# Kernel optimization log

Measured on AMD Instinct MI355X. Metric: run time of the kernel, lower is better.

The kernel has to match this reference:

```python
import jax, jax.numpy as jnp
import numpy as np

N = 131072      # total nodes
B = 512         # number of graphs
F_DIM = 512     # in_channels
H = F_DIM // 2  # score_net hidden
RATIO = 0.5
MARGIN = 0.5
TOPK_LOSS_WEIGHT = 0.2


def setup_inputs() -> dict:
    key = jax.random.key(0)
    k1, k2, k3 = jax.random.split(key, 3)
    x = jax.random.normal(k1, (N, F_DIM), dtype=jnp.float32)
    # sorted segment ids: equal-sized graphs of N // B nodes
    batch = (jnp.arange(N) // (N // B)).astype(jnp.int32)
    W1 = jax.random.normal(k2, (F_DIM, H), dtype=jnp.float32) / np.sqrt(F_DIM).astype(np.float32)
    b1 = jnp.zeros((H,), dtype=jnp.float32)
    W2 = jax.random.normal(k3, (H, 1), dtype=jnp.float32) / np.sqrt(H).astype(np.float32)
    b2 = jnp.zeros((1,), dtype=jnp.float32)
    return {"x": x, "batch": batch, "W1": W1, "b1": b1, "W2": W2, "b2": b2}


def reference(x, batch, W1, b1, W2, b2):
    # scores = score_net(x).squeeze(-1)   [N]
    scores = (jax.nn.relu(x @ W1 + b1) @ W2 + b2)[:, 0]

    # per-graph node counts and k = max(1, int(ratio * n_i))
    counts = jax.ops.segment_sum(jnp.ones((N,), dtype=scores.dtype), batch, num_segments=B)
    k = jnp.maximum(1, jnp.floor(RATIO * counts).astype(jnp.int32))  # [B]

    # segmented top-k via lexsort: sort by (batch asc, score desc)
    order = jnp.lexsort((-scores, batch))          # [N] permutation
    b_sorted = batch[order]
    starts = jnp.cumsum(counts) - counts           # exclusive-cumsum segment starts
    rank = jnp.arange(N, dtype=counts.dtype) - starts[b_sorted]  # rank within graph (0 = highest score)
    sel_sorted = rank < k[b_sorted].astype(counts.dtype)
    selected_mask = jnp.zeros((N,), dtype=bool).at[order].set(sel_sorted)

    # global_add_pool over selected nodes
    m = selected_mask.astype(x.dtype)
    x_pooled = jax.ops.segment_sum(x * m[:, None], batch, num_segments=B)  # [B, F]

    # margin regularization loss per graph
    sel_cnt = jax.ops.segment_sum(m, batch, num_segments=B)
    sel_sum = jax.ops.segment_sum(scores * m, batch, num_segments=B)
    tot_sum = jax.ops.segment_sum(scores, batch, num_segments=B)
    uns_cnt = counts - sel_cnt
    sel_mean = sel_sum / jnp.maximum(sel_cnt, 1.0)
    uns_mean = (tot_sum - sel_sum) / jnp.maximum(uns_cnt, 1.0)
    per_graph = jnp.where(uns_cnt > 0, jax.nn.relu(MARGIN - (sel_mean - uns_mean)), 0.0)
    topk_loss = per_graph.sum() / B * TOPK_LOSS_WEIGHT

    return x_pooled, topk_loss, selected_mask
```

## Files before the change

### kernel.cpp

```cpp
#include <hip/hip_runtime.h>

#define BGRAPHS 512
#define FDIM    512
#define HDIM    256
#define NPG     256
#define KSEL    128
#define STAGES  16
#define BSTAGE_SHORTS 16384
#define A_ROW   40
#define A_PLANE (NPG * A_ROW)

typedef __attribute__((ext_vector_type(8)))  _Float16 f16x8;
typedef __attribute__((ext_vector_type(8)))  short    s16x8;
typedef __attribute__((ext_vector_type(16))) float    f32x16;

__device__ __forceinline__ unsigned short f16_rne(float f, float* back) {
    _Float16 h = (_Float16)f;
    *back = (float)h;
    union { _Float16 h; unsigned short s; } cv; cv.h = h;
    return cv.s;
}

__global__ __launch_bounds__(256)
void split_w1_kernel(const float* __restrict__ W1, unsigned short* __restrict__ wsB)
{
    const int uid  = blockIdx.x * 256 + threadIdx.x;
    const int lane = uid & 63;
    int t = uid >> 6;
    const int nt = t & 7;  t >>= 3;
    const int p  = t & 1;  t >>= 1;
    const int q  = t & 1;
    const int s  = t >> 1;
    const int n  = nt * 32 + (lane & 31);
    const int k0 = s * 32 + q * 16 + (lane >> 5) * 8;

    s16x8 v;
    #pragma unroll
    for (int j = 0; j < 8; ++j) {
        float w = W1[(size_t)(k0 + j) * HDIM + n] * 1024.0f;
        float f1, f2;
        unsigned short h1 = f16_rne(w, &f1);
        unsigned short h2 = f16_rne(w - f1, &f2);
        v[j] = (short)(p ? h2 : h1);
    }
    *(s16x8*)(wsB + (size_t)uid * 8) = v;
}

__global__ __launch_bounds__(512, 2)
void fused_kernel(const float* __restrict__ x,
                  const unsigned short* __restrict__ wsB,
                  const float* __restrict__ b1, const float* __restrict__ W2,
                  const float* __restrict__ b2,
                  float* __restrict__ pooled, float* __restrict__ mask_out,
                  float* __restrict__ loss_per_g)
{
    __shared__ __attribute__((aligned(16))) unsigned char smem[147456];

    const int g    = blockIdx.x;
    const int tid  = threadIdx.x;
    const int lane = tid & 63;
    const int wv   = tid >> 6;
    const int wy   = wv & 3;
    const int wx   = wv >> 2;
    const int l31  = lane & 31;
    const int lh   = lane >> 5;

    const int c     = tid & 7;
    const int rbase = tid >> 3;
    const float* aptr = x + ((size_t)(g * NPG + rbase)) * FDIM + c * 4;

    f32x16 acc[2][4];
    #pragma unroll
    for (int a = 0; a < 2; ++a)
        #pragma unroll
        for (int b = 0; b < 4; ++b)
            #pragma unroll
            for (int rr = 0; rr < 16; ++rr) acc[a][b][rr] = 0.f;

    float4 aA0, aA1, aA2, aA3;
    float4 aB0, aB1, aB2, aB3;

#define GLL_B(S1) do {                                                          \
    const unsigned short* _src = wsB + (size_t)(S1) * BSTAGE_SHORTS;            \
    unsigned short* _dst = (unsigned short*)smem + ((S1) & 1) * BSTAGE_SHORTS;  \
    _Pragma("unroll")                                                           \
    for (int _i = 0; _i < 4; ++_i) {                                            \
        const int _u = _i * 512 + tid;                                          \
        __builtin_amdgcn_global_load_lds(                                       \
            (const __attribute__((address_space(1))) unsigned int*)(_src + (size_t)_u * 8), \
            (__attribute__((address_space(3))) unsigned int*)(_dst + _u * 8),   \
            16, 0, 0);                                                          \
    } } while (0)

#define LOAD_PF(P0,P1,P2,P3,S2) do {                                            \
    const float* _ap = aptr + (S2) * 32;                                        \
    P0 = *(const float4*)(_ap + 0 * 64 * FDIM);                                 \
    P1 = *(const float4*)(_ap + 1 * 64 * FDIM);                                 \
    P2 = *(const float4*)(_ap + 2 * 64 * FDIM);                                 \
    P3 = *(const float4*)(_ap + 3 * 64 * FDIM); } while (0)

#define CONV1(P,KK,BUF) do {                                                    \
    float _f[4] = {P.x, P.y, P.z, P.w};                                         \
    unsigned short _H[4], _M[4];                                                \
    _Pragma("unroll")                                                           \
    for (int _j = 0; _j < 4; ++_j) {                                            \
        float _b1v, _b2v;                                                       \
        float _xs = _f[_j] * 64.0f;                            \
        _H[_j] = f16_rne(_xs, &_b1v);                                           \
        _M[_j] = f16_rne(_xs - _b1v, &_b2v);                                    \
        (void)_b2v;                                                             \
    }                                                                           \
    unsigned short* _pl = (unsigned short*)(smem + 65536 + (BUF) * 40960)       \
                          + (rbase + 64 * (KK)) * A_ROW + c * 4;                \
    uint2 _uH, _uM;                                                             \
    _uH.x = (unsigned)_H[0] | ((unsigned)_H[1] << 16);                          \
    _uH.y = (unsigned)_H[2] | ((unsigned)_H[3] << 16);                          \
    _uM.x = (unsigned)_M[0] | ((unsigned)_M[1] << 16);                          \
    _uM.y = (unsigned)_M[2] | ((unsigned)_M[3] << 16);                          \
    *(uint2*)_pl = _uH;                                                         \
    *(uint2*)(_pl + A_PLANE) = _uM;                                             \
    } while (0)

#define CONVERT_A(P0,P1,P2,P3,BUF) do {                                         \
    CONV1(P0, 0, BUF); CONV1(P1, 1, BUF);                                       \
    CONV1(P2, 2, BUF); CONV1(P3, 3, BUF); } while (0)

#define COMPUTE(BUF) do {                                                       \
    const f16x8* _bfp = (const f16x8*)(smem + (BUF) * (BSTAGE_SHORTS * 2));     \
    const unsigned short* _aB = (const unsigned short*)(smem + 65536 + (BUF) * 40960); \
    _Pragma("unroll")                                                           \
    for (int _q = 0; _q < 2; ++_q) {                                            \
        const int _a0 = (wy * 64 + l31) * A_ROW + _q * 16 + lh * 8;             \
        const int _a1 = _a0 + 32 * A_ROW;                                       \
        f16x8 A0h = *(const f16x8*)(_aB + _a0);                                 \
        f16x8 A0m = *(const f16x8*)(_aB + A_PLANE + _a0);                       \
        f16x8 A1h = *(const f16x8*)(_aB + _a1);                                 \
        f16x8 A1m = *(const f16x8*)(_aB + A_PLANE + _a1);                       \
        _Pragma("unroll")                                                       \
        for (int _nt = 0; _nt < 4; ++_nt) {                                     \
            const int _nn = wx * 4 + _nt;                                       \
            f16x8 Bh = _bfp[((_q * 2 + 0) * 8 + _nn) * 64 + lane];              \
            f16x8 Bm = _bfp[((_q * 2 + 1) * 8 + _nn) * 64 + lane];              \
            acc[0][_nt] = __builtin_amdgcn_mfma_f32_32x32x16_f16(A0h, Bh, acc[0][_nt], 0, 0, 0); \
            acc[1][_nt] = __builtin_amdgcn_mfma_f32_32x32x16_f16(A1h, Bh, acc[1][_nt], 0, 0, 0); \
            acc[0][_nt] = __builtin_amdgcn_mfma_f32_32x32x16_f16(A0m, Bh, acc[0][_nt], 0, 0, 0); \
            acc[1][_nt] = __builtin_amdgcn_mfma_f32_32x32x16_f16(A1m, Bh, acc[1][_nt], 0, 0, 0); \
            acc[0][_nt] = __builtin_amdgcn_mfma_f32_32x32x16_f16(A0h, Bm, acc[0][_nt], 0, 0, 0); \
            acc[1][_nt] = __builtin_amdgcn_mfma_f32_32x32x16_f16(A1h, Bm, acc[1][_nt], 0, 0, 0); \
        }                                                                       \
    } } while (0)

    LOAD_PF(aA0, aA1, aA2, aA3, 0);
    GLL_B(0);
    CONVERT_A(aA0, aA1, aA2, aA3, 0);
    LOAD_PF(aA0, aA1, aA2, aA3, 1);
    __syncthreads();

    for (int s = 0; s < STAGES; s += 2) {
        if (s < STAGES - 1) GLL_B(s + 1);
        if (s < STAGES - 2) LOAD_PF(aB0, aB1, aB2, aB3, s + 2);
        COMPUTE(0);
        if (s < STAGES - 1) CONVERT_A(aA0, aA1, aA2, aA3, 1);
        __syncthreads();

        if (s + 1 < STAGES - 1) GLL_B(s + 2);
        if (s + 1 < STAGES - 2) LOAD_PF(aA0, aA1, aA2, aA3, s + 3);
        COMPUTE(1);
        if (s + 1 < STAGES - 1) CONVERT_A(aB0, aB1, aB2, aB3, 0);
        __syncthreads();
    }

    float* Sp   = (float*)smem;
    float* sv   = Sp + 2 * NPG;
    int*   selr = (int*)(sv + NPG);
    float* redT = (float*)(selr + KSEL);
    float* redS = redT + NPG;

    float bb[4], ww[4];
    #pragma unroll
    for (int nt = 0; nt < 4; ++nt) {
        const int cc = wx * 128 + nt * 32 + l31;
        bb[nt] = b1[cc];
        ww[nt] = W2[cc];
    }
    const float unscale = 1.0f / 65536.0f;
    #pragma unroll
    for (int mt = 0; mt < 2; ++mt) {
        float pr[16];
        #pragma unroll
        for (int rr = 0; rr < 16; ++rr) pr[rr] = 0.f;
        #pragma unroll
        for (int nt = 0; nt < 4; ++nt)
            #pragma unroll
            for (int rr = 0; rr < 16; ++rr) {
                float h = fmaf(acc[mt][nt][rr], unscale, bb[nt]);
                h = h > 0.f ? h : 0.f;
                pr[rr] = fmaf(h, ww[nt], pr[rr]);
            }
        #pragma unroll
        for (int mask = 1; mask <= 16; mask <<= 1)
            #pragma unroll
            for (int rr = 0; rr < 16; ++rr)
                pr[rr] += __shfl_xor(pr[rr], mask);
        if (l31 == 0) {
            #pragma unroll
            for (int rr = 0; rr < 16; ++rr) {
                const int row = wy * 64 + mt * 32 + (rr & 3) + 8 * (rr >> 2) + 4 * lh;
                Sp[wx * NPG + row] = pr[rr];
            }
        }
    }
    __syncthreads();

    float sc = 0.f;
    if (tid < NPG) {
        sc = b2[0] + Sp[tid] + Sp[NPG + tid];
        sv[tid] = sc;
    }
    __syncthreads();

    if (tid < NPG) {
        int rank = 0;
        for (int j = 0; j < NPG; ++j) {
            const float sj = sv[j];
            rank += (sj > sc || (sj == sc && j < tid)) ? 1 : 0;
        }
        const bool sel = rank < KSEL;
        mask_out[g * NPG + tid] = sel ? 1.0f : 0.0f;
        if (sel) selr[rank] = tid;
        redT[tid] = sc;
        redS[tid] = sel ? sc : 0.f;
    }
    __syncthreads();

    for (int off = 128; off > 0; off >>= 1) {
        if (tid < off) { redT[tid] += redT[tid + off]; redS[tid] += redS[tid + off]; }
        __syncthreads();
    }
    if (tid == 0) {
        const float tot = redT[0], ssum = redS[0];
        const float sel_mean = ssum * (1.0f / KSEL);
        const float uns_mean = (tot - ssum) * (1.0f / (NPG - KSEL));
        const float v = 0.5f - (sel_mean - uns_mean);
        loss_per_g[g] = v > 0.f ? v : 0.f;
    }

    const int col = tid;
    const float* __restrict__ xg = x + (size_t)g * NPG * FDIM;
    float a0 = 0.f, a1 = 0.f, a2 = 0.f, a3 = 0.f;
    float a4 = 0.f, a5 = 0.f, a6 = 0.f, a7 = 0.f;
    #pragma unroll 2
    for (int n = 0; n < KSEL; n += 8) {
        a0 += xg[(size_t)selr[n + 0] * FDIM + col];
        a1 += xg[(size_t)selr[n + 1] * FDIM + col];
        a2 += xg[(size_t)selr[n + 2] * FDIM + col];
        a3 += xg[(size_t)selr[n + 3] * FDIM + col];
        a4 += xg[(size_t)selr[n + 4] * FDIM + col];
        a5 += xg[(size_t)selr[n + 5] * FDIM + col];
        a6 += xg[(size_t)selr[n + 6] * FDIM + col];
        a7 += xg[(size_t)selr[n + 7] * FDIM + col];
    }
    pooled[g * FDIM + col] = ((a0 + a1) + (a2 + a3)) + ((a4 + a5) + (a6 + a7));

#undef GLL_B
#undef LOAD_PF
#undef CONV1
#undef CONVERT_A
#undef COMPUTE
}

__global__ __launch_bounds__(256)
void loss_kernel(const float* __restrict__ loss_per_g, float* __restrict__ out_loss)
{
    __shared__ float red[256];
    const int t = threadIdx.x;
    red[t] = loss_per_g[t] + loss_per_g[t + 256];
    __syncthreads();
    for (int off = 128; off > 0; off >>= 1) {
        if (t < off) red[t] += red[t + off];
        __syncthreads();
    }
    if (t == 0) out_loss[0] = red[0] * (0.2f / BGRAPHS);
}

extern "C" void kernel_launch(void* const* d_in, const int* in_sizes, int n_in,
                              void* d_out, int out_size, void* d_ws, size_t ws_size,
                              hipStream_t stream)
{
    const float* x  = (const float*)d_in[0];
    const float* W1 = (const float*)d_in[2];
    const float* b1 = (const float*)d_in[3];
    const float* W2 = (const float*)d_in[4];
    const float* b2 = (const float*)d_in[5];

    float* out    = (float*)d_out;
    float* pooled = out;
    float* loss   = out + BGRAPHS * FDIM;
    float* mask   = loss + 1;

    float* loss_g       = (float*)d_ws;
    unsigned short* wsB = (unsigned short*)((char*)d_ws + 4096);

    split_w1_kernel<<<128, 256, 0, stream>>>(W1, wsB);
    fused_kernel<<<BGRAPHS, 512, 0, stream>>>(x, wsB, b1, W2, b2,
                                              pooled, mask, loss_g);
    loss_kernel<<<1, 256, 0, stream>>>(loss_g, loss);
}
```

Measured before the change: 417.3 us.

## Split fused kernel into half-graph GEMM and separate select/pool kernels

```diff
diff --git a/kernel.cpp b/kernel.cpp
--- a/kernel.cpp
+++ b/kernel.cpp
@@ -5,10 +5,10 @@
 #define HDIM    256
 #define NPG     256
 #define KSEL    128
-#define STAGES  16
-#define BSTAGE_SHORTS 16384
-#define A_ROW   40
-#define A_PLANE (NPG * A_ROW)
+#define STAGES  32
+#define BSTAGE_SHORTS 8192
+#define A_ROW   24
+#define A_PLANE (128 * A_ROW)
 
 typedef __attribute__((ext_vector_type(8)))  _Float16 f16x8;
 typedef __attribute__((ext_vector_type(8)))  short    s16x8;
@@ -29,10 +29,9 @@
     int t = uid >> 6;
     const int nt = t & 7;  t >>= 3;
     const int p  = t & 1;  t >>= 1;
-    const int q  = t & 1;
-    const int s  = t >> 1;
+    const int s  = t;
     const int n  = nt * 32 + (lane & 31);
-    const int k0 = s * 32 + q * 16 + (lane >> 5) * 8;
+    const int k0 = s * 16 + (lane >> 5) * 8;
 
     s16x8 v;
     #pragma unroll
@@ -46,45 +45,45 @@
     *(s16x8*)(wsB + (size_t)uid * 8) = v;
 }
 
-__global__ __launch_bounds__(512, 2)
-void fused_kernel(const float* __restrict__ x,
-                  const unsigned short* __restrict__ wsB,
-                  const float* __restrict__ b1, const float* __restrict__ W2,
-                  const float* __restrict__ b2,
-                  float* __restrict__ pooled, float* __restrict__ mask_out,
-                  float* __restrict__ loss_per_g)
-{
-    __shared__ __attribute__((aligned(16))) unsigned char smem[147456];
-
-    const int g    = blockIdx.x;
+__global__ __launch_bounds__(512, 4)
+void gemm_kernel(const float* __restrict__ x,
+                 const unsigned short* __restrict__ wsB,
+                 const float* __restrict__ b1, const float* __restrict__ W2,
+                 const float* __restrict__ b2,
+                 float* __restrict__ scores_out)
+{
+    __shared__ __attribute__((aligned(16))) unsigned char smem[57344];
+
+    const int bid  = blockIdx.x;
+    const int g    = bid >> 1;
+    const int rh   = bid & 1;
     const int tid  = threadIdx.x;
     const int lane = tid & 63;
     const int wv   = tid >> 6;
-    const int wy   = wv & 3;
-    const int wx   = wv >> 2;
+    const int wy   = wv & 1;
+    const int wx   = wv >> 1;
     const int l31  = lane & 31;
     const int lh   = lane >> 5;
 
-    const int c     = tid & 7;
-    const int rbase = tid >> 3;
-    const float* aptr = x + ((size_t)(g * NPG + rbase)) * FDIM + c * 4;
-
-    f32x16 acc[2][4];
+    const int arow  = tid >> 2;
+    const int achk  = tid & 3;
+    const float* aptr = x + ((size_t)(g * NPG + rh * 128 + arow)) * FDIM + achk * 4;
+
+    f32x16 acc[2][2];
     #pragma unroll
     for (int a = 0; a < 2; ++a)
         #pragma unroll
-        for (int b = 0; b < 4; ++b)
+        for (int b = 0; b < 2; ++b)
             #pragma unroll
             for (int rr = 0; rr < 16; ++rr) acc[a][b][rr] = 0.f;
 
-    float4 aA0, aA1, aA2, aA3;
-    float4 aB0, aB1, aB2, aB3;
+    float4 aA, aB;
 
 #define GLL_B(S1) do {                                                          \
     const unsigned short* _src = wsB + (size_t)(S1) * BSTAGE_SHORTS;            \
     unsigned short* _dst = (unsigned short*)smem + ((S1) & 1) * BSTAGE_SHORTS;  \
     _Pragma("unroll")                                                           \
-    for (int _i = 0; _i < 4; ++_i) {                                            \
+    for (int _i = 0; _i < 2; ++_i) {                                            \
         const int _u = _i * 512 + tid;                                          \
         __builtin_amdgcn_global_load_lds(                                       \
             (const __attribute__((address_space(1))) unsigned int*)(_src + (size_t)_u * 8), \
@@ -92,14 +91,9 @@
             16, 0, 0);                                                          \
     } } while (0)
 
-#define LOAD_PF(P0,P1,P2,P3,S2) do {                                            \
-    const float* _ap = aptr + (S2) * 32;                                        \
-    P0 = *(const float4*)(_ap + 0 * 64 * FDIM);                                 \
-    P1 = *(const float4*)(_ap + 1 * 64 * FDIM);                                 \
-    P2 = *(const float4*)(_ap + 2 * 64 * FDIM);                                 \
-    P3 = *(const float4*)(_ap + 3 * 64 * FDIM); } while (0)
-
-#define CONV1(P,KK,BUF) do {                                                    \
+#define LOAD_PF(P,S2) do { P = *(const float4*)(aptr + (S2) * 16); } while (0)
+
+#define CONVERT_A(P,BUF) do {                                                   \
     float _f[4] = {P.x, P.y, P.z, P.w};                                         \
     unsigned short _H[4], _M[4];                                                \
     _Pragma("unroll")                                                           \
@@ -110,8 +104,8 @@
         _M[_j] = f16_rne(_xs - _b1v, &_b2v);                                    \
         (void)_b2v;                                                             \
     }                                                                           \
-    unsigned short* _pl = (unsigned short*)(smem + 65536 + (BUF) * 40960)       \
-                          + (rbase + 64 * (KK)) * A_ROW + c * 4;                \
+    unsigned short* _pl = (unsigned short*)(smem + 32768 + (BUF) * 12288)       \
+                          + arow * A_ROW + achk * 4;                            \
     uint2 _uH, _uM;                                                             \
     _uH.x = (unsigned)_H[0] | ((unsigned)_H[1] << 16);                          \
     _uH.y = (unsigned)_H[2] | ((unsigned)_H[3] << 16);                          \
@@ -121,65 +115,59 @@
     *(uint2*)(_pl + A_PLANE) = _uM;                                             \
     } while (0)
 
-#define CONVERT_A(P0,P1,P2,P3,BUF) do {                                         \
-    CONV1(P0, 0, BUF); CONV1(P1, 1, BUF);                                       \
-    CONV1(P2, 2, BUF); CONV1(P3, 3, BUF); } while (0)
-
 #define COMPUTE(BUF) do {                                                       \
     const f16x8* _bfp = (const f16x8*)(smem + (BUF) * (BSTAGE_SHORTS * 2));     \
-    const unsigned short* _aB = (const unsigned short*)(smem + 65536 + (BUF) * 40960); \
-    _Pragma("unroll")                                                           \
-    for (int _q = 0; _q < 2; ++_q) {                                            \
-        const int _a0 = (wy * 64 + l31) * A_ROW + _q * 16 + lh * 8;             \
-        const int _a1 = _a0 + 32 * A_ROW;                                       \
-        f16x8 A0h = *(const f16x8*)(_aB + _a0);                                 \
-        f16x8 A0m = *(const f16x8*)(_aB + A_PLANE + _a0);                       \
-        f16x8 A1h = *(const f16x8*)(_aB + _a1);                                 \
-        f16x8 A1m = *(const f16x8*)(_aB + A_PLANE + _a1);                       \
-        _Pragma("unroll")                                                       \
-        for (int _nt = 0; _nt < 4; ++_nt) {                                     \
-            const int _nn = wx * 4 + _nt;                                       \
-            f16x8 Bh = _bfp[((_q * 2 + 0) * 8 + _nn) * 64 + lane];              \
-            f16x8 Bm = _bfp[((_q * 2 + 1) * 8 + _nn) * 64 + lane];              \
-            acc[0][_nt] = __builtin_amdgcn_mfma_f32_32x32x16_f16(A0h, Bh, acc[0][_nt], 0, 0, 0); \
-            acc[1][_nt] = __builtin_amdgcn_mfma_f32_32x32x16_f16(A1h, Bh, acc[1][_nt], 0, 0, 0); \
-            acc[0][_nt] = __builtin_amdgcn_mfma_f32_32x32x16_f16(A0m, Bh, acc[0][_nt], 0, 0, 0); \
-            acc[1][_nt] = __builtin_amdgcn_mfma_f32_32x32x16_f16(A1m, Bh, acc[1][_nt], 0, 0, 0); \
-            acc[0][_nt] = __builtin_amdgcn_mfma_f32_32x32x16_f16(A0h, Bm, acc[0][_nt], 0, 0, 0); \
-            acc[1][_nt] = __builtin_amdgcn_mfma_f32_32x32x16_f16(A1h, Bm, acc[1][_nt], 0, 0, 0); \
-        }                                                                       \
-    } } while (0)
-
-    LOAD_PF(aA0, aA1, aA2, aA3, 0);
+    const unsigned short* _aB = (const unsigned short*)(smem + 32768 + (BUF) * 12288); \
+    const int _a0 = (wy * 64 + l31) * A_ROW + lh * 8;                           \
+    f16x8 A0h = *(const f16x8*)(_aB + _a0);                                     \
+    f16x8 A0m = *(const f16x8*)(_aB + A_PLANE + _a0);                           \
+    f16x8 A1h = *(const f16x8*)(_aB + _a0 + 32 * A_ROW);                        \
+    f16x8 A1m = *(const f16x8*)(_aB + A_PLANE + _a0 + 32 * A_ROW);              \
+    const int _nn = wx * 2;                                                     \
+    f16x8 Bh0 = _bfp[(0 * 8 + _nn + 0) * 64 + lane];                            \
+    f16x8 Bh1 = _bfp[(0 * 8 + _nn + 1) * 64 + lane];                            \
+    f16x8 Bm0 = _bfp[(1 * 8 + _nn + 0) * 64 + lane];                            \
+    f16x8 Bm1 = _bfp[(1 * 8 + _nn + 1) * 64 + lane];                            \
+    acc[0][0] = __builtin_amdgcn_mfma_f32_32x32x16_f16(A0h, Bh0, acc[0][0], 0, 0, 0); \
+    acc[0][1] = __builtin_amdgcn_mfma_f32_32x32x16_f16(A0h, Bh1, acc[0][1], 0, 0, 0); \
+    acc[1][0] = __builtin_amdgcn_mfma_f32_32x32x16_f16(A1h, Bh0, acc[1][0], 0, 0, 0); \
+    acc[1][1] = __builtin_amdgcn_mfma_f32_32x32x16_f16(A1h, Bh1, acc[1][1], 0, 0, 0); \
+    acc[0][0] = __builtin_amdgcn_mfma_f32_32x32x16_f16(A0m, Bh0, acc[0][0], 0, 0, 0); \
+    acc[0][1] = __builtin_amdgcn_mfma_f32_32x32x16_f16(A0m, Bh1, acc[0][1], 0, 0, 0); \
+    acc[1][0] = __builtin_amdgcn_mfma_f32_32x32x16_f16(A1m, Bh0, acc[1][0], 0, 0, 0); \
+    acc[1][1] = __builtin_amdgcn_mfma_f32_32x32x16_f16(A1m, Bh1, acc[1][1], 0, 0, 0); \
+    acc[0][0] = __builtin_amdgcn_mfma_f32_32x32x16_f16(A0h, Bm0, acc[0][0], 0, 0, 0); \
+    acc[0][1] = __builtin_amdgcn_mfma_f32_32x32x16_f16(A0h, Bm1, acc[0][1], 0, 0, 0); \
+    acc[1][0] = __builtin_amdgcn_mfma_f32_32x32x16_f16(A1h, Bm0, acc[1][0], 0, 0, 0); \
+    acc[1][1] = __builtin_amdgcn_mfma_f32_32x32x16_f16(A1h, Bm1, acc[1][1], 0, 0, 0); \
+    } while (0)
+
+    LOAD_PF(aA, 0);
     GLL_B(0);
-    CONVERT_A(aA0, aA1, aA2, aA3, 0);
-    LOAD_PF(aA0, aA1, aA2, aA3, 1);
+    CONVERT_A(aA, 0);
+    LOAD_PF(aA, 1);
     __syncthreads();
 
     for (int s = 0; s < STAGES; s += 2) {
         if (s < STAGES - 1) GLL_B(s + 1);
-        if (s < STAGES - 2) LOAD_PF(aB0, aB1, aB2, aB3, s + 2);
+        if (s < STAGES - 2) LOAD_PF(aB, s + 2);
         COMPUTE(0);
-        if (s < STAGES - 1) CONVERT_A(aA0, aA1, aA2, aA3, 1);
+        if (s < STAGES - 1) CONVERT_A(aA, 1);
         __syncthreads();
 
         if (s + 1 < STAGES - 1) GLL_B(s + 2);
-        if (s + 1 < STAGES - 2) LOAD_PF(aA0, aA1, aA2, aA3, s + 3);
+        if (s + 1 < STAGES - 2) LOAD_PF(aA, s + 3);
         COMPUTE(1);
-        if (s + 1 < STAGES - 1) CONVERT_A(aB0, aB1, aB2, aB3, 0);
+        if (s + 1 < STAGES - 1) CONVERT_A(aB, 0);
         __syncthreads();
     }
 
-    float* Sp   = (float*)smem;
-    float* sv   = Sp + 2 * NPG;
-    int*   selr = (int*)(sv + NPG);
-    float* redT = (float*)(selr + KSEL);
-    float* redS = redT + NPG;
-
-    float bb[4], ww[4];
+    float* scr = (float*)smem;
+
+    float bb[2], ww[2];
     #pragma unroll
-    for (int nt = 0; nt < 4; ++nt) {
-        const int cc = wx * 128 + nt * 32 + l31;
+    for (int nt = 0; nt < 2; ++nt) {
+        const int cc = wx * 64 + nt * 32 + l31;
         bb[nt] = b1[cc];
         ww[nt] = W2[cc];
     }
@@ -190,7 +178,7 @@
         #pragma unroll
         for (int rr = 0; rr < 16; ++rr) pr[rr] = 0.f;
         #pragma unroll
-        for (int nt = 0; nt < 4; ++nt)
+        for (int nt = 0; nt < 2; ++nt)
             #pragma unroll
             for (int rr = 0; rr < 16; ++rr) {
                 float h = fmaf(acc[mt][nt][rr], unscale, bb[nt]);
@@ -206,15 +194,40 @@
             #pragma unroll
             for (int rr = 0; rr < 16; ++rr) {
                 const int row = wy * 64 + mt * 32 + (rr & 3) + 8 * (rr >> 2) + 4 * lh;
-                Sp[wx * NPG + row] = pr[rr];
+                scr[wx * 128 + row] = pr[rr];
             }
         }
     }
     __syncthreads();
 
+    if (tid < 128) {
+        const float s = b2[0] + scr[tid] + scr[128 + tid] + scr[256 + tid] + scr[384 + tid];
+        scores_out[g * NPG + rh * 128 + tid] = s;
+    }
+
+#undef GLL_B
+#undef LOAD_PF
+#undef CONVERT_A
+#undef COMPUTE
+}
+
+__global__ __launch_bounds__(512)
+void select_pool_kernel(const float* __restrict__ x,
+                        float* __restrict__ scores_mask,
+                        float* __restrict__ pooled,
+                        float* __restrict__ loss_per_g)
+{
+    __shared__ float sv[NPG];
+    __shared__ int   selr[KSEL];
+    __shared__ float redT[NPG];
+    __shared__ float redS[NPG];
+
+    const int g   = blockIdx.x;
+    const int tid = threadIdx.x;
+
     float sc = 0.f;
     if (tid < NPG) {
-        sc = b2[0] + Sp[tid] + Sp[NPG + tid];
+        sc = scores_mask[g * NPG + tid];
         sv[tid] = sc;
     }
     __syncthreads();
@@ -226,7 +239,7 @@
             rank += (sj > sc || (sj == sc && j < tid)) ? 1 : 0;
         }
         const bool sel = rank < KSEL;
-        mask_out[g * NPG + tid] = sel ? 1.0f : 0.0f;
+        scores_mask[g * NPG + tid] = sel ? 1.0f : 0.0f;
         if (sel) selr[rank] = tid;
         redT[tid] = sc;
         redS[tid] = sel ? sc : 0.f;
@@ -261,12 +274,6 @@
         a7 += xg[(size_t)selr[n + 7] * FDIM + col];
     }
     pooled[g * FDIM + col] = ((a0 + a1) + (a2 + a3)) + ((a4 + a5) + (a6 + a7));
-
-#undef GLL_B
-#undef LOAD_PF
-#undef CONV1
-#undef CONVERT_A
-#undef COMPUTE
 }
 
 __global__ __launch_bounds__(256)
@@ -302,7 +309,7 @@
     unsigned short* wsB = (unsigned short*)((char*)d_ws + 4096);
 
     split_w1_kernel<<<128, 256, 0, stream>>>(W1, wsB);
-    fused_kernel<<<BGRAPHS, 512, 0, stream>>>(x, wsB, b1, W2, b2,
-                                              pooled, mask, loss_g);
+    gemm_kernel<<<2 * BGRAPHS, 512, 0, stream>>>(x, wsB, b1, W2, b2, mask);
+    select_pool_kernel<<<BGRAPHS, 512, 0, stream>>>(x, mask, pooled, loss_g);
     loss_kernel<<<1, 256, 0, stream>>>(loss_g, loss);
 }
```

Measured after the change: 426.2 us. 1.02x slower.
